# Optimization experiments

Measured on AMD Instinct MI355X. Metric: run time of the kernel, lower is better.

Reference implementation:

```python
import jax, jax.numpy as jnp
import numpy as np

B, C, D, E, ES, TOPK = 8, 4096, 1024, 16, 256, 4096

def setup_inputs() -> dict:
    key = jax.random.key(0)
    k1, k2, k3, k4 = jax.random.split(key, 4)
    x = jax.random.normal(k1, (B, C, D), dtype=jnp.float32)
    gate = jax.random.normal(k2, (C, E), dtype=jnp.float32) / np.sqrt(D)
    lin1_weight = jax.random.normal(k3, (D, E, ES), dtype=jnp.float32) / np.sqrt(D)
    lin2_weight = jax.random.normal(k4, (E, ES, D), dtype=jnp.float32) / np.sqrt(ES)
    return {"x": x, "gate": gate, "lin1_weight": lin1_weight, "lin2_weight": lin2_weight, "topk": TOPK}

def reference(x, gate, lin1_weight, lin2_weight, topk):
    b, c, d = x.shape
    e = gate.shape[1]
    n_tokens = b * c
    # faithful to original einsum: sum x over dmodel, elementwise-mult by gate[c, e]
    gate_out = jnp.einsum('bcd,ce->bce', x, gate)            # [b, c, e]
    gate_out = jnp.transpose(gate_out, (2, 0, 1)).reshape(e, n_tokens)
    gate_out = jax.nn.softmax(gate_out, axis=1)              # softmax over tokens per expert
    topk_values, topk_indices = jax.lax.top_k(gate_out, topk)  # [e, k]
    xf = x.reshape(n_tokens, d)
    flat_idx = topk_indices.reshape(-1)
    gathered = xf[flat_idx].reshape(e, topk, d)              # dispatch
    h = jax.nn.relu(jnp.einsum('ekd,des->eks', gathered, lin1_weight))
    out = jnp.einsum('eks,esd->ekd', h, lin2_weight)
    out = out * topk_values[..., None]                       # weight by gate probs
    z = jnp.zeros_like(xf).at[flat_idx].add(out.reshape(-1, d))  # scatter-add combine
    return z.reshape(b, c, d)
```

## Files before the change

kernel.cpp:

```cpp
#include <hip/hip_runtime.h>
#include <hip/hip_bf16.h>

#define BB 8
#define CC 4096
#define DD 1024
#define EE 16
#define ESS 256
#define KSEL 4096
#define NTOK (BB*CC)

typedef short bf16x8 __attribute__((ext_vector_type(8)));
typedef float f32x4 __attribute__((ext_vector_type(4)));

__device__ __forceinline__ short f2bf(float f) {
  unsigned u = __float_as_uint(f);
  u += 0x7FFFu + ((u >> 16) & 1u);
  return (short)(u >> 16);
}
__device__ __forceinline__ float bf2f(short s) {
  return __uint_as_float(((unsigned)(unsigned short)s) << 16);
}

#define ASG __attribute__((address_space(1)))
#define ASL __attribute__((address_space(3)))
__device__ __forceinline__ void gl_lds16(void* l, const void* g) {
  __builtin_amdgcn_global_load_lds((ASG const unsigned*)g, (ASL unsigned*)l, 16, 0, 0);
}

__global__ void k_logits(const float* __restrict__ x, const float* __restrict__ gate,
                         float* __restrict__ logits, short* __restrict__ xb) {
  int wid = threadIdx.x >> 6, lane = threadIdx.x & 63;
  int t = blockIdx.x * 4 + wid;
  const float4* xr = reinterpret_cast<const float4*>(x + (size_t)t * DD);
  short4* xw = reinterpret_cast<short4*>(xb + (size_t)t * DD);
  float s = 0.f;
#pragma unroll
  for (int i = 0; i < 4; ++i) {
    float4 v = xr[lane + 64 * i];
    s += v.x + v.y + v.z + v.w;
    short4 p;
    p.x = f2bf(v.x); p.y = f2bf(v.y); p.z = f2bf(v.z); p.w = f2bf(v.w);
    xw[lane + 64 * i] = p;
  }
#pragma unroll
  for (int off = 32; off; off >>= 1) s += __shfl_xor(s, off);
  if (lane < EE) {
    int c = t & (CC - 1);
    logits[(size_t)lane * NTOK + t] = s * gate[c * EE + lane];
  }
}

__global__ __launch_bounds__(1024) void k_select(
    const float* __restrict__ logits, int* __restrict__ sel_idx,
    float* __restrict__ sel_val, int* __restrict__ inv) {
  int e = blockIdx.x;
  const float* L = logits + (size_t)e * NTOK;
  __shared__ unsigned whist[16][256];
  __shared__ unsigned chist[256];
  __shared__ float red[1024];
  __shared__ float sh_mx, sh_sm;
  __shared__ unsigned sh_prefix, sh_kth, sh_ngt;
  __shared__ unsigned wtg[16], wtq[16];
  __shared__ unsigned base_gt, base_eq;
  int tid = threadIdx.x, wid = tid >> 6, lane = tid & 63;

  unsigned prefix = 0, kth = KSEL, n_gt = 0;
  float mloc = -3.4e38f, sloc = 0.f;
  for (int pass = 3; pass >= 0; --pass) {
    for (int i = tid; i < 16 * 256; i += 1024) ((unsigned*)whist)[i] = 0;
    __syncthreads();
    float mxl = (pass == 2) ? sh_mx : 0.f;
    unsigned shift = pass * 8;
    unsigned pmask = (pass == 3) ? 0u : (0xFFFFFFFFu << ((pass + 1) * 8));
    for (int t = tid; t < NTOK; t += 1024) {
      float lv = L[t];
      unsigned u = __float_as_uint(lv);
      unsigned key = (u & 0x80000000u) ? ~u : (u | 0x80000000u);
      if (pass == 3) mloc = fmaxf(mloc, lv);
      if (pass == 2) sloc += expf(lv - mxl);
      if ((key & pmask) == prefix) atomicAdd(&whist[wid][(key >> shift) & 255], 1u);
    }
    __syncthreads();
    if (tid < 256) {
      unsigned s = 0;
#pragma unroll
      for (int w = 0; w < 16; ++w) s += whist[w][tid];
      chist[tid] = s;
    }
    if (pass == 3) red[tid] = mloc;
    if (pass == 2) red[tid] = sloc;
    __syncthreads();
    if (pass == 3) {
      for (int s2 = 512; s2; s2 >>= 1) {
        if (tid < s2) red[tid] = fmaxf(red[tid], red[tid + s2]);
        __syncthreads();
      }
      if (tid == 0) sh_mx = red[0];
    }
    if (pass == 2) {
      for (int s2 = 512; s2; s2 >>= 1) {
        if (tid < s2) red[tid] += red[tid + s2];
        __syncthreads();
      }
      if (tid == 0) sh_sm = red[0];
    }
    if (tid == 0) {
      unsigned cum = 0; int d = 255;
      for (; d >= 0; --d) {
        if (cum + chist[d] >= kth) break;
        cum += chist[d];
      }
      sh_ngt = n_gt + cum;
      sh_kth = kth - cum;
      sh_prefix = prefix | ((unsigned)d << shift);
    }
    __syncthreads();
    prefix = sh_prefix; kth = sh_kth; n_gt = sh_ngt;
    __syncthreads();
  }
  unsigned tau = prefix;
  unsigned n_tie = KSEL - n_gt;
  float mx = sh_mx, sm = sh_sm;

  if (tid == 0) { base_gt = 0; base_eq = 0; }
  __syncthreads();
  for (int t0 = 0; t0 < NTOK; t0 += 1024) {
    int t = t0 + tid;
    float lv = L[t];
    unsigned u = __float_as_uint(lv);
    unsigned key = (u & 0x80000000u) ? ~u : (u | 0x80000000u);
    bool g = key > tau, q = key == tau;
    unsigned long long bg = __ballot(g), bq = __ballot(q);
    unsigned long long lm = (1ull << lane) - 1ull;
    unsigned pg = __popcll(bg & lm), pq = __popcll(bq & lm);
    if (lane == 63) { wtg[wid] = pg + (g ? 1u : 0u); wtq[wid] = pq + (q ? 1u : 0u); }
    __syncthreads();
    unsigned og = base_gt, oq = base_eq;
    for (int w2 = 0; w2 < wid; ++w2) { og += wtg[w2]; oq += wtq[w2]; }
    unsigned slot = 0xFFFFFFFFu;
    if (g) slot = og + pg;
    else if (q) {
      unsigned r = oq + pq;
      if (r < n_tie) slot = n_gt + r;
    }
    if (slot != 0xFFFFFFFFu) {
      sel_idx[(size_t)e * KSEL + slot] = t;
      sel_val[(size_t)e * KSEL + slot] = expf(lv - mx) / sm;
      inv[(size_t)t * EE + e] = e * KSEL + (int)slot;
    }
    __syncthreads();
    if (tid == 0) {
      unsigned sg = 0, sq = 0;
#pragma unroll
      for (int w2 = 0; w2 < 16; ++w2) { sg += wtg[w2]; sq += wtq[w2]; }
      base_gt += sg; base_eq += sq;
    }
    __syncthreads();
  }
}

__global__ void k_transpose(const float* __restrict__ src, short* __restrict__ dst,
                            int R, int C) {
  __shared__ float tile[64][65];
  int c0 = blockIdx.x * 64, r0 = blockIdx.y * 64, b = blockIdx.z;
  const float* S = src + (size_t)b * R * C;
  short* Dp = dst + (size_t)b * R * C;
  int tx = threadIdx.x & 63, ty = threadIdx.x >> 6;
#pragma unroll
  for (int i = 0; i < 16; ++i) {
    int r = ty + 4 * i;
    tile[r][tx] = S[(size_t)(r0 + r) * C + c0 + tx];
  }
  __syncthreads();
#pragma unroll
  for (int i = 0; i < 16; ++i) {
    int cR = ty + 4 * i;
    Dp[(size_t)(c0 + cR) * R + r0 + tx] = f2bf(tile[tx][cR]);
  }
}

__global__ __launch_bounds__(512, 4) void k_gemm1(
    const short* __restrict__ xb, const short* __restrict__ W1T,
    const int* __restrict__ sel_idx, const float* __restrict__ sel_val,
    short* __restrict__ H) {
  int bid = blockIdx.x;
  int m0 = ((bid >> 3) & 31) * 128;
  int e = (bid & 7) + ((bid >> 8) << 3);
  __shared__ bf16x8 As8[128 * 8];
  __shared__ bf16x8 Bs8[256 * 8];
  int tid = threadIdx.x, lane = tid & 63, wid = tid >> 6;
  int wr = wid >> 2, wc = wid & 3;
  const int* idxE = sel_idx + (size_t)e * KSEL;
  f32x4 acc[4][4] = {};

  int rowA = tid >> 3, sA = tid & 7;
  int xk = rowA & 7;
  const short* aSrc0 = xb + (size_t)idxE[m0 + rowA] * DD + (sA ^ xk) * 8;
  const short* aSrc1 = xb + (size_t)idxE[m0 + rowA + 64] * DD + (sA ^ xk) * 8;
  const short* wBase = W1T + (size_t)e * ESS * DD + (size_t)rowA * DD + (sA ^ xk) * 8;

  for (int kt = 0; kt < DD / 64; ++kt) {
    int kofs = kt * 64;
    gl_lds16(&As8[tid], aSrc0 + kofs);
    gl_lds16(&As8[512 + tid], aSrc1 + kofs);
#pragma unroll
    for (int j = 0; j < 4; ++j)
      gl_lds16(&Bs8[j * 512 + tid], wBase + (size_t)(64 * j) * DD + kofs);
    __syncthreads();
    bf16x8 af[4][2];
#pragma unroll
    for (int mg = 0; mg < 4; ++mg) {
      int row = wr * 64 + mg * 16 + (lane & 15);
#pragma unroll
      for (int h = 0; h < 2; ++h) {
        int seg = h * 4 + (lane >> 4);
        af[mg][h] = As8[row * 8 + (seg ^ (row & 7))];
      }
    }
#pragma unroll
    for (int ng = 0; ng < 4; ++ng) {
      int rowb = wc * 64 + ng * 16 + (lane & 15);
      bf16x8 b0 = Bs8[rowb * 8 + (((lane >> 4) + 0) ^ (rowb & 7))];
      bf16x8 b1 = Bs8[rowb * 8 + (((lane >> 4) + 4) ^ (rowb & 7))];
#pragma unroll
      for (int mg = 0; mg < 4; ++mg) {
        acc[mg][ng] = __builtin_amdgcn_mfma_f32_16x16x32_bf16(af[mg][0], b0, acc[mg][ng], 0, 0, 0);
        acc[mg][ng] = __builtin_amdgcn_mfma_f32_16x16x32_bf16(af[mg][1], b1, acc[mg][ng], 0, 0, 0);
      }
    }
    __syncthreads();
  }
#pragma unroll
  for (int mg = 0; mg < 4; ++mg) {
#pragma unroll
    for (int r = 0; r < 4; ++r) {
      int ml = wr * 64 + mg * 16 + (lane >> 4) * 4 + r;
      float v = sel_val[(size_t)e * KSEL + m0 + ml];
#pragma unroll
      for (int ng = 0; ng < 4; ++ng) {
        float o = fmaxf(acc[mg][ng][r], 0.f) * v;
        H[((size_t)(e * KSEL + m0 + ml)) * ESS + wc * 64 + ng * 16 + (lane & 15)] = f2bf(o);
      }
    }
  }
}

template <int COMBINE>
__global__ __launch_bounds__(512, 4) void k_gemm2(
    const short* __restrict__ H, const short* __restrict__ W2T,
    const int* __restrict__ sel_idx, float* __restrict__ z, short* __restrict__ out) {
  int bid = blockIdx.x;
  int p = (bid & 7) + ((bid >> 8) << 3);
  int m0 = ((bid >> 3) & 31) * 128;
  int n0 = (p & 3) * 256;
  int e = p >> 2;
  __shared__ bf16x8 As8[128 * 8];
  __shared__ bf16x8 Bs8[256 * 8];
  int tid = threadIdx.x, lane = tid & 63, wid = tid >> 6;
  int wr = wid >> 2, wc = wid & 3;
  f32x4 acc[4][4] = {};

  int rowA = tid >> 3, sA = tid & 7;
  int xk = rowA & 7;
  const short* hBase = H + (size_t)(e * KSEL + m0 + rowA) * ESS + (sA ^ xk) * 8;
  const short* w2Base = W2T + (size_t)(e * DD + n0 + rowA) * ESS + (sA ^ xk) * 8;

  for (int kt = 0; kt < ESS / 64; ++kt) {
    int kofs = kt * 64;
    gl_lds16(&As8[tid], hBase + kofs);
    gl_lds16(&As8[512 + tid], hBase + (size_t)64 * ESS + kofs);
#pragma unroll
    for (int j = 0; j < 4; ++j)
      gl_lds16(&Bs8[j * 512 + tid], w2Base + (size_t)(64 * j) * ESS + kofs);
    __syncthreads();
    bf16x8 af[4][2];
#pragma unroll
    for (int mg = 0; mg < 4; ++mg) {
      int row = wr * 64 + mg * 16 + (lane & 15);
#pragma unroll
      for (int h = 0; h < 2; ++h) {
        int seg = h * 4 + (lane >> 4);
        af[mg][h] = As8[row * 8 + (seg ^ (row & 7))];
      }
    }
#pragma unroll
    for (int ng = 0; ng < 4; ++ng) {
      int rowb = wc * 64 + ng * 16 + (lane & 15);
      bf16x8 b0 = Bs8[rowb * 8 + (((lane >> 4) + 0) ^ (rowb & 7))];
      bf16x8 b1 = Bs8[rowb * 8 + (((lane >> 4) + 4) ^ (rowb & 7))];
#pragma unroll
      for (int mg = 0; mg < 4; ++mg) {
        acc[mg][ng] = __builtin_amdgcn_mfma_f32_16x16x32_bf16(af[mg][0], b0, acc[mg][ng], 0, 0, 0);
        acc[mg][ng] = __builtin_amdgcn_mfma_f32_16x16x32_bf16(af[mg][1], b1, acc[mg][ng], 0, 0, 0);
      }
    }
    __syncthreads();
  }
#pragma unroll
  for (int mg = 0; mg < 4; ++mg) {
#pragma unroll
    for (int r = 0; r < 4; ++r) {
      int ml = wr * 64 + mg * 16 + (lane >> 4) * 4 + r;
      if (COMBINE) {
        short* orow = out + ((size_t)(e * KSEL + m0 + ml)) * DD + n0 + wc * 64 + (lane & 15);
#pragma unroll
        for (int ng = 0; ng < 4; ++ng) orow[ng * 16] = f2bf(acc[mg][ng][r]);
      } else {
        int token = sel_idx[(size_t)e * KSEL + m0 + ml];
        float* zr = z + (size_t)token * DD + n0 + wc * 64 + (lane & 15);
#pragma unroll
        for (int ng = 0; ng < 4; ++ng) atomicAdd(zr + ng * 16, acc[mg][ng][r]);
      }
    }
  }
}

__global__ void k_combine(const short* __restrict__ out, const int* __restrict__ inv,
                          float* __restrict__ z) {
  int wid = threadIdx.x >> 6, lane = threadIdx.x & 63;
  int t = blockIdx.x * 4 + wid;
  int g[16];
  const int4* iv4 = reinterpret_cast<const int4*>(inv + (size_t)t * EE);
#pragma unroll
  for (int q = 0; q < 4; ++q) {
    int4 v = iv4[q];
    g[4 * q] = v.x; g[4 * q + 1] = v.y; g[4 * q + 2] = v.z; g[4 * q + 3] = v.w;
  }
  float acc[16] = {};
#pragma unroll
  for (int e = 0; e < EE; ++e) {
    if (g[e] < 0) continue;
    const uint4* rp = reinterpret_cast<const uint4*>(out + (size_t)g[e] * DD + lane * 16);
    uint4 v0 = rp[0], v1 = rp[1];
    const short* s0 = reinterpret_cast<const short*>(&v0);
    const short* s1 = reinterpret_cast<const short*>(&v1);
#pragma unroll
    for (int i = 0; i < 8; ++i) acc[i] += bf2f(s0[i]);
#pragma unroll
    for (int i = 0; i < 8; ++i) acc[8 + i] += bf2f(s1[i]);
  }
  float4* zw = reinterpret_cast<float4*>(z + (size_t)t * DD + lane * 16);
#pragma unroll
  for (int i = 0; i < 4; ++i) {
    float4 o; o.x = acc[4 * i]; o.y = acc[4 * i + 1]; o.z = acc[4 * i + 2]; o.w = acc[4 * i + 3];
    zw[i] = o;
  }
}

extern "C" void kernel_launch(void* const* d_in, const int* in_sizes, int n_in,
                              void* d_out, int out_size, void* d_ws, size_t ws_size,
                              hipStream_t stream) {
  (void)in_sizes; (void)n_in;
  const float* x = (const float*)d_in[0];
  const float* gate = (const float*)d_in[1];
  const float* lin1 = (const float*)d_in[2];
  const float* lin2 = (const float*)d_in[3];
  float* z = (float*)d_out;

  char* ws = (char*)d_ws;
  size_t off = 0;
  auto alloc = [&](size_t bytes) -> void* {
    off = (off + 255) & ~(size_t)255;
    void* p = ws + off;
    off += bytes;
    return p;
  };
  float* logits = (float*)alloc((size_t)EE * NTOK * 4);
  int* sidx = (int*)alloc((size_t)EE * KSEL * 4);
  float* sval = (float*)alloc((size_t)EE * KSEL * 4);
  int* inv = (int*)alloc((size_t)NTOK * EE * 4);
  short* W1T = (short*)alloc((size_t)EE * ESS * DD * 2);
  short* W2T = (short*)alloc((size_t)EE * DD * ESS * 2);
  short* H = (short*)alloc((size_t)EE * KSEL * ESS * 2);
  short* xb = (short*)alloc((size_t)NTOK * DD * 2);
  size_t out_bytes = (size_t)EE * KSEL * DD * 2;
  bool combine = (off + 256 + out_bytes) <= ws_size;
  short* outbuf = combine ? (short*)alloc(out_bytes) : nullptr;

  k_transpose<<<dim3(64, 16, 1), 256, 0, stream>>>(lin1, W1T, DD, EE * ESS);
  k_transpose<<<dim3(16, 4, 16), 256, 0, stream>>>(lin2, W2T, ESS, DD);
  k_logits<<<NTOK / 4, 256, 0, stream>>>(x, gate, logits, xb);
  hipMemsetAsync(inv, 0xFF, (size_t)NTOK * EE * 4, stream);
  k_select<<<EE, 1024, 0, stream>>>(logits, sidx, sval, inv);
  k_gemm1<<<512, 512, 0, stream>>>(xb, W1T, sidx, sval, H);
  if (combine) {
    k_gemm2<1><<<2048, 512, 0, stream>>>(H, W2T, sidx, z, outbuf);
    k_combine<<<NTOK / 4, 256, 0, stream>>>(outbuf, inv, z);
  } else {
    hipMemsetAsync(d_out, 0, (size_t)out_size * sizeof(float), stream);
    k_gemm2<0><<<2048, 512, 0, stream>>>(H, W2T, sidx, z, nullptr);
  }
}
```

Baseline: 351.4 us.

## Split top-k selection into parallel histogram, pick, and atomic compaction kernels

Replaces the single 16-block radix-select kernel with three kernels. A 128-block pass builds a global 16-bit-prefix histogram and partial exp sums, a per-expert pick kernel refines the threshold with two 8-bit passes, and a 128-block compaction assigns slots with global atomics. This targets the low parallelism and four serial passes of the old select, which ran only 16 blocks on a large GPU. In exchange the selected tokens now land in nondeterministic slot order, and the softmax is computed without subtracting the max, which risks overflow for large logits.

```diff
diff --git a/kernel.cpp b/kernel.cpp
--- a/kernel.cpp
+++ b/kernel.cpp
@@ -12,6 +12,8 @@
 typedef short bf16x8 __attribute__((ext_vector_type(8)));
 typedef float f32x4 __attribute__((ext_vector_type(4)));
 
+struct PickRes { unsigned tau; unsigned n_gt; unsigned n_tie; float sm; };
+
 __device__ __forceinline__ short f2bf(float f) {
   unsigned u = __float_as_uint(f);
   u += 0x7FFFu + ((u >> 16) & 1u);
@@ -19,6 +21,10 @@
 }
 __device__ __forceinline__ float bf2f(short s) {
   return __uint_as_float(((unsigned)(unsigned short)s) << 16);
+}
+__device__ __forceinline__ unsigned f2key(float f) {
+  unsigned u = __float_as_uint(f);
+  return (u & 0x80000000u) ? ~u : (u | 0x80000000u);
 }
 
 #define ASG __attribute__((address_space(1)))
@@ -50,112 +56,127 @@
   }
 }
 
-__global__ __launch_bounds__(1024) void k_select(
-    const float* __restrict__ logits, int* __restrict__ sel_idx,
-    float* __restrict__ sel_val, int* __restrict__ inv) {
+__global__ __launch_bounds__(1024) void k_hist(const float* __restrict__ logits,
+                                               unsigned* __restrict__ ghist,
+                                               float* __restrict__ separt) {
+  int e = blockIdx.x & 15, seg = blockIdx.x >> 4;
+  const float* L = logits + (size_t)e * NTOK + seg * 4096;
+  unsigned* Hh = ghist + (size_t)e * 65536;
+  int tid = threadIdx.x;
+  float sl = 0.f;
+#pragma unroll
+  for (int i = 0; i < 4; ++i) {
+    float lv = L[tid + 1024 * i];
+    atomicAdd(&Hh[f2key(lv) >> 16], 1u);
+    sl += expf(lv);
+  }
+  __shared__ float red[1024];
+  red[tid] = sl; __syncthreads();
+  for (int s2 = 512; s2; s2 >>= 1) {
+    if (tid < s2) red[tid] += red[tid + s2];
+    __syncthreads();
+  }
+  if (tid == 0) separt[e * 8 + seg] = red[0];
+}
+
+__global__ __launch_bounds__(1024) void k_pick(const unsigned* __restrict__ ghist,
+                                               const float* __restrict__ logits,
+                                               const float* __restrict__ separt,
+                                               PickRes* __restrict__ pres) {
   int e = blockIdx.x;
+  const unsigned* Hh = ghist + (size_t)e * 65536;
   const float* L = logits + (size_t)e * NTOK;
-  __shared__ unsigned whist[16][256];
-  __shared__ unsigned chist[256];
-  __shared__ float red[1024];
-  __shared__ float sh_mx, sh_sm;
-  __shared__ unsigned sh_prefix, sh_kth, sh_ngt;
-  __shared__ unsigned wtg[16], wtq[16];
-  __shared__ unsigned base_gt, base_eq;
-  int tid = threadIdx.x, wid = tid >> 6, lane = tid & 63;
-
-  unsigned prefix = 0, kth = KSEL, n_gt = 0;
-  float mloc = -3.4e38f, sloc = 0.f;
-  for (int pass = 3; pass >= 0; --pass) {
-    for (int i = tid; i < 16 * 256; i += 1024) ((unsigned*)whist)[i] = 0;
-    __syncthreads();
-    float mxl = (pass == 2) ? sh_mx : 0.f;
-    unsigned shift = pass * 8;
-    unsigned pmask = (pass == 3) ? 0u : (0xFFFFFFFFu << ((pass + 1) * 8));
-    for (int t = tid; t < NTOK; t += 1024) {
-      float lv = L[t];
-      unsigned u = __float_as_uint(lv);
-      unsigned key = (u & 0x80000000u) ? ~u : (u | 0x80000000u);
-      if (pass == 3) mloc = fmaxf(mloc, lv);
-      if (pass == 2) sloc += expf(lv - mxl);
-      if ((key & pmask) == prefix) atomicAdd(&whist[wid][(key >> shift) & 255], 1u);
-    }
-    __syncthreads();
-    if (tid < 256) {
-      unsigned s = 0;
-#pragma unroll
-      for (int w = 0; w < 16; ++w) s += whist[w][tid];
-      chist[tid] = s;
-    }
-    if (pass == 3) red[tid] = mloc;
-    if (pass == 2) red[tid] = sloc;
-    __syncthreads();
-    if (pass == 3) {
-      for (int s2 = 512; s2; s2 >>= 1) {
-        if (tid < s2) red[tid] = fmaxf(red[tid], red[tid + s2]);
-        __syncthreads();
-      }
-      if (tid == 0) sh_mx = red[0];
-    }
-    if (pass == 2) {
-      for (int s2 = 512; s2; s2 >>= 1) {
-        if (tid < s2) red[tid] += red[tid + s2];
-        __syncthreads();
-      }
-      if (tid == 0) sh_sm = red[0];
-    }
-    if (tid == 0) {
-      unsigned cum = 0; int d = 255;
-      for (; d >= 0; --d) {
-        if (cum + chist[d] >= kth) break;
-        cum += chist[d];
-      }
-      sh_ngt = n_gt + cum;
-      sh_kth = kth - cum;
-      sh_prefix = prefix | ((unsigned)d << shift);
-    }
-    __syncthreads();
-    prefix = sh_prefix; kth = sh_kth; n_gt = sh_ngt;
-    __syncthreads();
-  }
-  unsigned tau = prefix;
-  unsigned n_tie = KSEL - n_gt;
-  float mx = sh_mx, sm = sh_sm;
-
-  if (tid == 0) { base_gt = 0; base_eq = 0; }
-  __syncthreads();
-  for (int t0 = 0; t0 < NTOK; t0 += 1024) {
-    int t = t0 + tid;
+  int tid = threadIdx.x;
+  __shared__ unsigned u0[1024], u1[1024];
+  __shared__ unsigned hist256[256];
+  __shared__ unsigned sh_b16, sh_ngt, sh_kth;
+  __shared__ unsigned sh_p24, sh_ngt2, sh_kth2;
+
+  unsigned cs = 0;
+  for (int j = 0; j < 64; ++j) cs += Hh[tid * 64 + j];
+  u0[tid] = cs; __syncthreads();
+  unsigned* src = u0; unsigned* dst = u1;
+  for (int d2 = 1; d2 < 1024; d2 <<= 1) {
+    unsigned v = src[tid] + ((tid + d2 < 1024) ? src[tid + d2] : 0u);
+    dst[tid] = v; __syncthreads();
+    unsigned* tmp = src; src = dst; dst = tmp;
+  }
+  unsigned kth0 = KSEL;
+  unsigned above = (tid < 1023) ? src[tid + 1] : 0u;
+  if (above < kth0 && kth0 <= src[tid]) {
+    unsigned cum = above;
+    for (int j = 63; j >= 0; --j) {
+      unsigned h = Hh[tid * 64 + j];
+      if (cum + h >= kth0) { sh_b16 = (unsigned)(tid * 64 + j); sh_ngt = cum; sh_kth = kth0 - cum; break; }
+      cum += h;
+    }
+  }
+  __syncthreads();
+  unsigned p16 = sh_b16, ngt1 = sh_ngt, kth1 = sh_kth;
+
+  if (tid < 256) hist256[tid] = 0;
+  __syncthreads();
+  for (int t = tid; t < NTOK; t += 1024) {
+    unsigned key = f2key(L[t]);
+    if ((key >> 16) == p16) atomicAdd(&hist256[(key >> 8) & 255], 1u);
+  }
+  __syncthreads();
+  if (tid == 0) {
+    unsigned cum = 0; int d = 255;
+    for (; d >= 0; --d) { unsigned h = hist256[d]; if (cum + h >= kth1) break; cum += h; }
+    sh_p24 = (p16 << 8) | (unsigned)d;
+    sh_ngt2 = ngt1 + cum;
+    sh_kth2 = kth1 - cum;
+  }
+  __syncthreads();
+  unsigned p24 = sh_p24, ngt2 = sh_ngt2, kth2 = sh_kth2;
+
+  if (tid < 256) hist256[tid] = 0;
+  __syncthreads();
+  for (int t = tid; t < NTOK; t += 1024) {
+    unsigned key = f2key(L[t]);
+    if ((key >> 8) == p24) atomicAdd(&hist256[key & 255], 1u);
+  }
+  __syncthreads();
+  if (tid == 0) {
+    unsigned cum = 0; int d = 255;
+    for (; d >= 0; --d) { unsigned h = hist256[d]; if (cum + h >= kth2) break; cum += h; }
+    unsigned tau = (p24 << 8) | (unsigned)d;
+    unsigned n_gt = ngt2 + cum;
+    float sm = 0.f;
+    for (int j = 0; j < 8; ++j) sm += separt[e * 8 + j];
+    PickRes pr; pr.tau = tau; pr.n_gt = n_gt; pr.n_tie = KSEL - n_gt; pr.sm = sm;
+    pres[e] = pr;
+  }
+}
+
+__global__ __launch_bounds__(1024) void k_compact(const float* __restrict__ logits,
+                                                  const PickRes* __restrict__ pres,
+                                                  int* __restrict__ sel_idx,
+                                                  float* __restrict__ sel_val,
+                                                  int* __restrict__ inv,
+                                                  unsigned* __restrict__ ctrs) {
+  int e = blockIdx.x & 15, seg = blockIdx.x >> 4;
+  PickRes pr = pres[e];
+  const float* L = logits + (size_t)e * NTOK;
+  int t0 = seg * 4096;
+  int tid = threadIdx.x;
+#pragma unroll
+  for (int i = 0; i < 4; ++i) {
+    int t = t0 + tid + 1024 * i;
     float lv = L[t];
-    unsigned u = __float_as_uint(lv);
-    unsigned key = (u & 0x80000000u) ? ~u : (u | 0x80000000u);
-    bool g = key > tau, q = key == tau;
-    unsigned long long bg = __ballot(g), bq = __ballot(q);
-    unsigned long long lm = (1ull << lane) - 1ull;
-    unsigned pg = __popcll(bg & lm), pq = __popcll(bq & lm);
-    if (lane == 63) { wtg[wid] = pg + (g ? 1u : 0u); wtq[wid] = pq + (q ? 1u : 0u); }
-    __syncthreads();
-    unsigned og = base_gt, oq = base_eq;
-    for (int w2 = 0; w2 < wid; ++w2) { og += wtg[w2]; oq += wtq[w2]; }
+    unsigned key = f2key(lv);
     unsigned slot = 0xFFFFFFFFu;
-    if (g) slot = og + pg;
-    else if (q) {
-      unsigned r = oq + pq;
-      if (r < n_tie) slot = n_gt + r;
+    if (key > pr.tau) slot = atomicAdd(&ctrs[e * 2], 1u);
+    else if (key == pr.tau) {
+      unsigned r = atomicAdd(&ctrs[e * 2 + 1], 1u);
+      if (r < pr.n_tie) slot = pr.n_gt + r;
     }
     if (slot != 0xFFFFFFFFu) {
       sel_idx[(size_t)e * KSEL + slot] = t;
-      sel_val[(size_t)e * KSEL + slot] = expf(lv - mx) / sm;
+      sel_val[(size_t)e * KSEL + slot] = expf(lv) / pr.sm;
       inv[(size_t)t * EE + e] = e * KSEL + (int)slot;
     }
-    __syncthreads();
-    if (tid == 0) {
-      unsigned sg = 0, sq = 0;
-#pragma unroll
-      for (int w2 = 0; w2 < 16; ++w2) { sg += wtg[w2]; sq += wtq[w2]; }
-      base_gt += sg; base_eq += sq;
-    }
-    __syncthreads();
   }
 }
 
@@ -377,11 +398,20 @@
   bool combine = (off + 256 + out_bytes) <= ws_size;
   short* outbuf = combine ? (short*)alloc(out_bytes) : nullptr;
 
+  unsigned* ghist = (unsigned*)H;
+  float* separt = (float*)((char*)H + (size_t)EE * 65536 * 4);
+  PickRes* pres = (PickRes*)((char*)separt + 1024);
+  unsigned* ctrs = (unsigned*)((char*)pres + 1024);
+
   k_transpose<<<dim3(64, 16, 1), 256, 0, stream>>>(lin1, W1T, DD, EE * ESS);
   k_transpose<<<dim3(16, 4, 16), 256, 0, stream>>>(lin2, W2T, ESS, DD);
   k_logits<<<NTOK / 4, 256, 0, stream>>>(x, gate, logits, xb);
   hipMemsetAsync(inv, 0xFF, (size_t)NTOK * EE * 4, stream);
-  k_select<<<EE, 1024, 0, stream>>>(logits, sidx, sval, inv);
+  hipMemsetAsync(ghist, 0, (size_t)EE * 65536 * 4, stream);
+  hipMemsetAsync(ctrs, 0, 128, stream);
+  k_hist<<<128, 1024, 0, stream>>>(logits, ghist, separt);
+  k_pick<<<EE, 1024, 0, stream>>>(ghist, logits, separt, pres);
+  k_compact<<<128, 1024, 0, stream>>>(logits, pres, sidx, sval, inv, ctrs);
   k_gemm1<<<512, 512, 0, stream>>>(xb, W1T, sidx, sval, H);
   if (combine) {
     k_gemm2<1><<<2048, 512, 0, stream>>>(H, W2T, sidx, z, outbuf);
```

After: 364.6 us. +3.7%, slower.
